# Performance work log

Hardware: AMD Instinct MI355X
Metric: run time of the kernel (lower is better)

The kernel has to match this reference:

```python
import jax, jax.numpy as jnp
import numpy as np

EPS = 1e-08


def setup_inputs() -> dict:
    key = jax.random.key(0)
    k_x, k_w1, k_b1, k_w2, k_b2 = jax.random.split(key, 5)
    B, C, T = 64, 64, 4000
    x = jax.random.normal(k_x, (B, C, T, 1), dtype=jnp.float32)
    # 1x1 Conv2D with in_channels=1, out_channels=8 -> weight is an 8-vector + bias
    w1 = jax.random.normal(k_w1, (8,), dtype=jnp.float32) * 0.5
    b1 = jax.random.normal(k_b1, (8,), dtype=jnp.float32) * 0.1
    w2 = jax.random.normal(k_w2, (8,), dtype=jnp.float32) * 0.5
    b2 = jax.random.normal(k_b2, (8,), dtype=jnp.float32) * 0.1
    # gamma is initialized to 0 in the module (residual identity at init);
    # use a nonzero value so the attention path is exercised numerically.
    gamma = jnp.float32(0.5)
    return {"x": x, "w1": w1, "b1": b1, "w2": w2, "b2": b2, "gamma": gamma}


def reference(x, w1, b1, w2, b2, gamma):
    B, C, T, _ = x.shape  # (B, num_ch, T, 1)
    # 1x1 conv with C_in=1: broadcast multiply-add, then flatten (T, 8) -> T*8
    q = (x * w1 + b1).reshape(B, C, T * 8)  # proj_query (B, C, T*8)
    k = (x * w2 + b2).reshape(B, C, T * 8)  # proj_key   (B, C, T*8)
    # energy = Q @ K^T  -> (B, C, C)
    energy = jnp.einsum('bcd,bed->bce', q, k)
    # custom min-max normalization along last axis, then softmax
    max_h = jnp.max(energy, axis=2, keepdims=True)
    min_h = jnp.min(energy, axis=2, keepdims=True)
    energy = (energy - min_h) / (max_h - min_h + EPS)
    attention = jax.nn.softmax(energy, axis=-1)
    xs = x[..., 0]  # squeeze last dim -> (B, C, T)
    # attention^T @ xs  (transpose_a=True)
    attended = jnp.einsum('bec,bet->bct', attention, xs)
    return gamma * attended[..., None] + x
```

## Files before the change

kernel.cpp:

```cpp
#include <hip/hip_runtime.h>

#define BB 64
#define CC 64
#define TT 4000

#define SLABS 8
#define TSLAB 250
#define SLABT (2 * TSLAB)
#define GP_PITCH 264

#define TPB 128
#define APITCH 72

#define GPART_ELEMS ((size_t)SLABS * BB * CC * CC)

typedef short short8 __attribute__((ext_vector_type(8)));
typedef float f32x16 __attribute__((ext_vector_type(16)));

__device__ __forceinline__ short f2bf(float f) {
    unsigned u = __float_as_uint(f);
    u = (u + 0x7FFFu + ((u >> 16) & 1u)) >> 16;
    return (short)u;
}
__device__ __forceinline__ float bfpair(unsigned u) {
    return __uint_as_float(u << 16) + __uint_as_float(u & 0xFFFF0000u);
}

__device__ __forceinline__ void stage_load(const float* __restrict__ xb, int t0,
                                           int g, int tid, float4 v[8]) {
    #pragma unroll
    for (int k = 0; k < 8; ++k) {
        const int i = tid + 256 * (g * 8 + k);
        const int row = i >> 6, tq = i & 63;
        float4 w = make_float4(0.f, 0.f, 0.f, 0.f);
        if (tq < 62) {
            w = *(const float4*)(xb + row * TT + t0 + 4 * tq);
        } else if (tq == 62) {
            const float* p = xb + row * TT + t0 + 248;
            w.x = p[0]; w.y = p[1];
        }
        v[k] = w;
    }
}
__device__ __forceinline__ void stage_write(short* xs, int g, int tid, const float4 v[8]) {
    #pragma unroll
    for (int k = 0; k < 8; ++k) {
        const int i = tid + 256 * (g * 8 + k);
        const int row = i >> 6, tq = i & 63;
        short4 sv;
        sv.x = f2bf(v[k].x); sv.y = f2bf(v[k].y);
        sv.z = f2bf(v[k].z); sv.w = f2bf(v[k].w);
        const int pc = (tq >> 1) ^ (row & 7);
        *(short4*)(xs + row * GP_PITCH + pc * 8 + (tq & 1) * 4) = sv;
    }
}
__device__ __forceinline__ float s_partial(const short* xs, int lane, int wave) {
    const short* rowp = xs + lane * GP_PITCH;
    float s = 0.f;
    #pragma unroll
    for (int j = 0; j < 8; ++j) {
        const int pc = (wave * 8 + j) ^ (lane & 7);
        uint2 u0 = *(const uint2*)(rowp + pc * 8);
        uint2 u1 = *(const uint2*)(rowp + pc * 8 + 4);
        s += bfpair(u0.x) + bfpair(u0.y) + bfpair(u1.x) + bfpair(u1.y);
    }
    return s;
}
__device__ __forceinline__ void mfma_tile(const short* xs, int r0, int c0,
                                          int m, int half, f32x16& acc) {
    #pragma unroll
    for (int ks = 0; ks < 16; ++ks) {
        const int ck = ks * 2 + half;
        short8 av = *(const short8*)(xs + (r0 + m) * GP_PITCH + (ck ^ (m & 7)) * 8);
        short8 bv = *(const short8*)(xs + (c0 + m) * GP_PITCH + (ck ^ (m & 7)) * 8);
        acc = __builtin_amdgcn_mfma_f32_32x32x16_bf16(av, bv, acc, 0, 0, 0);
    }
}

__global__ __launch_bounds__(256)
void gram_mfma(const float* __restrict__ x, float* __restrict__ G_part,
               float* __restrict__ S_part) {
    __shared__ short xs[2][CC * GP_PITCH];
    __shared__ float sred[4 * 64];
    const int b    = blockIdx.x / SLABS;
    const int slab = blockIdx.x % SLABS;
    const int tid  = threadIdx.x;
    const int lane = tid & 63;
    const int wave = tid >> 6;
    const float* xb = x + (size_t)b * CC * TT;

    const int r0 = (wave >> 1) * 32, c0 = (wave & 1) * 32;
    const int m = lane & 31, half = lane >> 5;
    f32x16 acc;
    #pragma unroll
    for (int z = 0; z < 16; ++z) acc[z] = 0.f;

    const int t0a = slab * SLABT, t0b = t0a + TSLAB;

    {
        float4 v[8];
        stage_load(xb, t0a, 0, tid, v);
        stage_write(xs[0], 0, tid, v);
        stage_load(xb, t0a, 1, tid, v);
        stage_write(xs[0], 1, tid, v);
    }
    __syncthreads();

    float4 p0[8], p1[8];
    stage_load(xb, t0b, 0, tid, p0);
    stage_load(xb, t0b, 1, tid, p1);

    float s_acc = s_partial(xs[0], lane, wave);
    mfma_tile(xs[0], r0, c0, m, half, acc);

    stage_write(xs[1], 0, tid, p0);
    stage_write(xs[1], 1, tid, p1);
    __syncthreads();

    s_acc += s_partial(xs[1], lane, wave);
    mfma_tile(xs[1], r0, c0, m, half, acc);

    sred[wave * 64 + lane] = s_acc;
    __syncthreads();
    if (tid < 64) {
        float s = sred[tid] + sred[64 + tid] + sred[128 + tid] + sred[192 + tid];
        S_part[(slab * BB + b) * CC + tid] = s;
    }
    float* gp = G_part + ((size_t)slab * BB + b) * (CC * CC);
    #pragma unroll
    for (int r = 0; r < 16; ++r) {
        const int row = (r & 3) + 8 * (r >> 2) + 4 * half;
        gp[(r0 + row) * CC + (c0 + m)] = acc[r];
    }
}

__global__ __launch_bounds__(256)
void softmax_apply(const float* __restrict__ x,
                   const float* __restrict__ w1, const float* __restrict__ b1,
                   const float* __restrict__ w2, const float* __restrict__ b2,
                   const float* __restrict__ G_part, const float* __restrict__ S_part,
                   const float* __restrict__ gamma, float* __restrict__ out) {
    __shared__ float Es[64 * 65];
    __shared__ short al[CC * APITCH];
    __shared__ float red[3 * 256];
    __shared__ float Sb[64];
    const int tid  = threadIdx.x;
    const int lane = tid & 63, wave = tid >> 6;
    const int b    = blockIdx.x & 63;
    const int slab = blockIdx.x >> 6;
    const float* xb = x + (size_t)b * CC * TT;
    const int m = lane & 31, half = lane >> 5;

    {
        #pragma unroll
        for (int j4 = 0; j4 < 4; ++j4) {
            const int jj = tid + 256 * j4;
            float4 s = make_float4(0.f, 0.f, 0.f, 0.f);
            #pragma unroll
            for (int sl = 0; sl < SLABS; ++sl) {
                const float4 g = *(const float4*)(G_part + ((size_t)sl * BB + b) * 4096 + 4 * jj);
                s.x += g.x; s.y += g.y; s.z += g.z; s.w += g.w;
            }
            const int row = jj >> 4, col = (jj & 15) * 4;
            float* e = Es + row * 65 + col;
            e[0] = s.x; e[1] = s.y; e[2] = s.z; e[3] = s.w;
        }
        if (tid < 64) {
            float s = 0.f;
            #pragma unroll
            for (int sl = 0; sl < SLABS; ++sl)
                s += S_part[(sl * BB + b) * CC + tid];
            Sb[tid] = s;
        }
        float A = 0.f, Bc = 0.f, Be = 0.f, Cc = 0.f;
        #pragma unroll
        for (int j = 0; j < 8; ++j) {
            float a1 = w1[j], a2 = w2[j], q1 = b1[j], q2 = b2[j];
            A += a1 * a2; Bc += a1 * q2; Be += q1 * a2; Cc += q1 * q2;
        }
        Cc *= (float)TT;
        __syncthreads();

        const int c = tid & 63, q = tid >> 6;
        const float sc = Sb[c];
        float ev[16], mn = 1e30f, mx = -1e30f;
        #pragma unroll
        for (int i = 0; i < 16; ++i) {
            const int e = 16 * q + i;
            float en = A * Es[c * 65 + e] + Bc * sc + Be * Sb[e] + Cc;
            ev[i] = en;
            mn = fminf(mn, en); mx = fmaxf(mx, en);
        }
        red[q * 64 + c] = mn; red[256 + q * 64 + c] = mx;
        __syncthreads();
        mn = fminf(fminf(red[c], red[64 + c]), fminf(red[128 + c], red[192 + c]));
        mx = fmaxf(fmaxf(red[256 + c], red[320 + c]), fmaxf(red[384 + c], red[448 + c]));
        const float ninv = 1.f / (mx - mn + 1e-8f);
        float pv[16], ls = 0.f;
        #pragma unroll
        for (int i = 0; i < 16; ++i) {
            float p = __expf((ev[i] - mn) * ninv);
            pv[i] = p; ls += p;
        }
        red[512 + q * 64 + c] = ls;
        __syncthreads();
        const float rinv = 1.f / (red[512 + c] + red[576 + c] + red[640 + c] + red[704 + c]);
        #pragma unroll
        for (int i = 0; i < 16; ++i)
            al[(16 * q + i) * APITCH + c] = f2bf(pv[i] * rinv);
        __syncthreads();
    }

    {
        const int c0 = (wave & 1) * 32;
        const int tb = (wave >> 1) * 64;
        short8 av[4];
        #pragma unroll
        for (int ks = 0; ks < 4; ++ks)
            av[ks] = *(const short8*)(al + (c0 + m) * APITCH + ks * 16 + 8 * half);

        const float gm = gamma[0];
        float* ob = out + (size_t)b * CC * TT;
        const int t0s = slab * SLABT;

        for (int it = 0; it < 4; ++it) {
            const int t0 = t0s + it * TPB;
            const int ta = t0 + tb + m;
            const int tc = ta + 32;
            f32x16 acc0, acc1;
            #pragma unroll
            for (int z = 0; z < 16; ++z) { acc0[z] = 0.f; acc1[z] = 0.f; }

            #pragma unroll
            for (int ks = 0; ks < 4; ++ks) {
                const int eb = ks * 16 + 8 * half;
                short8 bv0, bv1;
                #pragma unroll
                for (int j = 0; j < 8; ++j) {
                    const float xa = (ta < TT) ? xb[(eb + j) * TT + ta] : 0.f;
                    const float xc = (tc < TT) ? xb[(eb + j) * TT + tc] : 0.f;
                    bv0[j] = f2bf(xa);
                    bv1[j] = f2bf(xc);
                }
                acc0 = __builtin_amdgcn_mfma_f32_32x32x16_bf16(av[ks], bv0, acc0, 0, 0, 0);
                acc1 = __builtin_amdgcn_mfma_f32_32x32x16_bf16(av[ks], bv1, acc1, 0, 0, 0);
            }

            const int tl0 = it * TPB + tb + m;
            #pragma unroll
            for (int r = 0; r < 16; ++r) {
                const int row = (r & 3) + 8 * (r >> 2) + 4 * half;
                const int c = c0 + row;
                if (tl0 < SLABT)
                    ob[c * TT + ta] = gm * acc0[r] + xb[c * TT + ta];
                if (tl0 + 32 < SLABT)
                    ob[c * TT + tc] = gm * acc1[r] + xb[c * TT + tc];
            }
        }
    }
}

extern "C" void kernel_launch(void* const* d_in, const int* in_sizes, int n_in,
                              void* d_out, int out_size, void* d_ws, size_t ws_size,
                              hipStream_t stream) {
    const float* x  = (const float*)d_in[0];
    const float* w1 = (const float*)d_in[1];
    const float* b1 = (const float*)d_in[2];
    const float* w2 = (const float*)d_in[3];
    const float* b2 = (const float*)d_in[4];
    const float* gm = (const float*)d_in[5];
    float* out = (float*)d_out;

    float* G_part = (float*)d_ws;
    float* S_part = G_part + GPART_ELEMS;

    hipLaunchKernelGGL(gram_mfma, dim3(BB * SLABS), dim3(256), 0, stream,
                       x, G_part, S_part);
    hipLaunchKernelGGL(softmax_apply, dim3(BB * SLABS), dim3(256), 0, stream,
                       x, w1, b1, w2, b2, G_part, S_part, gm, out);
}
```

Baseline: 184.3 us.

## Stage x tiles in LDS with register prefetch and packed bf16 conversion

Result: faster. 157.3 us (-14.7%).

```diff
diff --git a/kernel.cpp b/kernel.cpp
--- a/kernel.cpp
+++ b/kernel.cpp
@@ -10,17 +10,24 @@
 #define GP_PITCH 264
 
 #define TPB 128
+#define XPITCH 132
 #define APITCH 72
 
 #define GPART_ELEMS ((size_t)SLABS * BB * CC * CC)
 
 typedef short short8 __attribute__((ext_vector_type(8)));
 typedef float f32x16 __attribute__((ext_vector_type(16)));
+typedef unsigned u32x4 __attribute__((ext_vector_type(4)));
 
 __device__ __forceinline__ short f2bf(float f) {
     unsigned u = __float_as_uint(f);
     u = (u + 0x7FFFu + ((u >> 16) & 1u)) >> 16;
     return (short)u;
+}
+__device__ __forceinline__ unsigned cvt_pk(float a, float b) {
+    unsigned r;
+    asm("v_cvt_pk_bf16_f32 %0, %1, %2" : "=v"(r) : "v"(a), "v"(b));
+    return r;
 }
 __device__ __forceinline__ float bfpair(unsigned u) {
     return __uint_as_float(u << 16) + __uint_as_float(u & 0xFFFF0000u);
@@ -47,11 +54,11 @@
     for (int k = 0; k < 8; ++k) {
         const int i = tid + 256 * (g * 8 + k);
         const int row = i >> 6, tq = i & 63;
-        short4 sv;
-        sv.x = f2bf(v[k].x); sv.y = f2bf(v[k].y);
-        sv.z = f2bf(v[k].z); sv.w = f2bf(v[k].w);
+        uint2 sv;
+        sv.x = cvt_pk(v[k].x, v[k].y);
+        sv.y = cvt_pk(v[k].z, v[k].w);
         const int pc = (tq >> 1) ^ (row & 7);
-        *(short4*)(xs + row * GP_PITCH + pc * 8 + (tq & 1) * 4) = sv;
+        *(uint2*)(xs + row * GP_PITCH + pc * 8 + (tq & 1) * 4) = sv;
     }
 }
 __device__ __forceinline__ float s_partial(const short* xs, int lane, int wave) {
@@ -141,6 +148,7 @@
                    const float* __restrict__ G_part, const float* __restrict__ S_part,
                    const float* __restrict__ gamma, float* __restrict__ out) {
     __shared__ float Es[64 * 65];
+    __shared__ float xsbuf[CC * XPITCH];
     __shared__ short al[CC * APITCH];
     __shared__ float red[3 * 256];
     __shared__ float Sb[64];
@@ -222,40 +230,70 @@
         const float gm = gamma[0];
         float* ob = out + (size_t)b * CC * TT;
         const int t0s = slab * SLABT;
+        const int ie = tid >> 5, ip = tid & 31;
+
+        float4 v[8];
+        #pragma unroll
+        for (int k = 0; k < 8; ++k) {
+            const int i = tid + 256 * k;
+            const int e = i >> 5, p = i & 31;
+            const int t = t0s + 4 * p;
+            v[k] = make_float4(0.f, 0.f, 0.f, 0.f);
+            if (t < TT) v[k] = *(const float4*)(xb + e * TT + t);
+        }
 
         for (int it = 0; it < 4; ++it) {
-            const int t0 = t0s + it * TPB;
-            const int ta = t0 + tb + m;
-            const int tc = ta + 32;
+            #pragma unroll
+            for (int k = 0; k < 8; ++k) {
+                const int i = tid + 256 * k;
+                const int e = i >> 5, p = i & 31;
+                *(float4*)(xsbuf + e * XPITCH + 4 * p) = v[k];
+            }
+            __syncthreads();
+            if (it < 3) {
+                const int t0n = t0s + (it + 1) * TPB;
+                #pragma unroll
+                for (int k = 0; k < 8; ++k) {
+                    const int i = tid + 256 * k;
+                    const int e = i >> 5, p = i & 31;
+                    const int t = t0n + 4 * p;
+                    v[k] = make_float4(0.f, 0.f, 0.f, 0.f);
+                    if (t < TT) v[k] = *(const float4*)(xb + e * TT + t);
+                }
+            }
+
             f32x16 acc0, acc1;
             #pragma unroll
             for (int z = 0; z < 16; ++z) { acc0[z] = 0.f; acc1[z] = 0.f; }
-
             #pragma unroll
             for (int ks = 0; ks < 4; ++ks) {
                 const int eb = ks * 16 + 8 * half;
-                short8 bv0, bv1;
+                u32x4 pk0, pk1;
                 #pragma unroll
-                for (int j = 0; j < 8; ++j) {
-                    const float xa = (ta < TT) ? xb[(eb + j) * TT + ta] : 0.f;
-                    const float xc = (tc < TT) ? xb[(eb + j) * TT + tc] : 0.f;
-                    bv0[j] = f2bf(xa);
-                    bv1[j] = f2bf(xc);
+                for (int j2 = 0; j2 < 4; ++j2) {
+                    const float* col = xsbuf + (eb + 2 * j2) * XPITCH;
+                    pk0[j2] = cvt_pk(col[tb + m],      col[XPITCH + tb + m]);
+                    pk1[j2] = cvt_pk(col[tb + 32 + m], col[XPITCH + tb + 32 + m]);
                 }
-                acc0 = __builtin_amdgcn_mfma_f32_32x32x16_bf16(av[ks], bv0, acc0, 0, 0, 0);
-                acc1 = __builtin_amdgcn_mfma_f32_32x32x16_bf16(av[ks], bv1, acc1, 0, 0, 0);
-            }
-
+                acc0 = __builtin_amdgcn_mfma_f32_32x32x16_bf16(
+                    av[ks], __builtin_bit_cast(short8, pk0), acc0, 0, 0, 0);
+                acc1 = __builtin_amdgcn_mfma_f32_32x32x16_bf16(
+                    av[ks], __builtin_bit_cast(short8, pk1), acc1, 0, 0, 0);
+            }
+
+            const int t0  = t0s + it * TPB;
+            const int ta  = t0 + tb + m, tc = ta + 32;
             const int tl0 = it * TPB + tb + m;
             #pragma unroll
             for (int r = 0; r < 16; ++r) {
                 const int row = (r & 3) + 8 * (r >> 2) + 4 * half;
                 const int c = c0 + row;
                 if (tl0 < SLABT)
-                    ob[c * TT + ta] = gm * acc0[r] + xb[c * TT + ta];
+                    ob[c * TT + ta] = gm * acc0[r] + xsbuf[c * XPITCH + tb + m];
                 if (tl0 + 32 < SLABT)
-                    ob[c * TT + tc] = gm * acc1[r] + xb[c * TT + tc];
-            }
+                    ob[c * TT + tc] = gm * acc1[r] + xsbuf[c * XPITCH + tb + 32 + m];
+            }
+            __syncthreads();
         }
     }
 }
```

## Fuse Gram, softmax and apply into one kernel with redundant per-block Gram

Applied to the files above, without the earlier changes.

After: 361.4 us. 96.1% more time.

```diff
diff --git a/kernel.cpp b/kernel.cpp
--- a/kernel.cpp
+++ b/kernel.cpp
@@ -4,15 +4,11 @@
 #define CC 64
 #define TT 4000
 
-#define SLABS 8
-#define TSLAB 250
-#define SLABT (2 * TSLAB)
+#define NSLAB 8
+#define NCHUNK 16
+#define TCH 250
 #define GP_PITCH 264
-
-#define TPB 128
 #define APITCH 72
-
-#define GPART_ELEMS ((size_t)SLABS * BB * CC * CC)
 
 typedef short short8 __attribute__((ext_vector_type(8)));
 typedef float f32x16 __attribute__((ext_vector_type(16)));
@@ -22,8 +18,16 @@
     u = (u + 0x7FFFu + ((u >> 16) & 1u)) >> 16;
     return (short)u;
 }
+__device__ __forceinline__ unsigned cvt_pk(float a, float b) {
+    unsigned r;
+    asm("v_cvt_pk_bf16_f32 %0, %1, %2" : "=v"(r) : "v"(a), "v"(b));
+    return r;
+}
 __device__ __forceinline__ float bfpair(unsigned u) {
     return __uint_as_float(u << 16) + __uint_as_float(u & 0xFFFF0000u);
+}
+__device__ __forceinline__ float bf2f(short s) {
+    return __uint_as_float(((unsigned)(unsigned short)s) << 16);
 }
 
 __device__ __forceinline__ void stage_load(const float* __restrict__ xb, int t0,
@@ -47,11 +51,11 @@
     for (int k = 0; k < 8; ++k) {
         const int i = tid + 256 * (g * 8 + k);
         const int row = i >> 6, tq = i & 63;
-        short4 sv;
-        sv.x = f2bf(v[k].x); sv.y = f2bf(v[k].y);
-        sv.z = f2bf(v[k].z); sv.w = f2bf(v[k].w);
+        uint2 sv;
+        sv.x = cvt_pk(v[k].x, v[k].y);
+        sv.y = cvt_pk(v[k].z, v[k].w);
         const int pc = (tq >> 1) ^ (row & 7);
-        *(short4*)(xs + row * GP_PITCH + pc * 8 + (tq & 1) * 4) = sv;
+        *(uint2*)(xs + row * GP_PITCH + pc * 8 + (tq & 1) * 4) = sv;
     }
 }
 __device__ __forceinline__ float s_partial(const short* xs, int lane, int wave) {
@@ -78,100 +82,59 @@
 }
 
 __global__ __launch_bounds__(256)
-void gram_mfma(const float* __restrict__ x, float* __restrict__ G_part,
-               float* __restrict__ S_part) {
-    __shared__ short xs[2][CC * GP_PITCH];
-    __shared__ float sred[4 * 64];
-    const int b    = blockIdx.x / SLABS;
-    const int slab = blockIdx.x % SLABS;
-    const int tid  = threadIdx.x;
-    const int lane = tid & 63;
-    const int wave = tid >> 6;
-    const float* xb = x + (size_t)b * CC * TT;
-
-    const int r0 = (wave >> 1) * 32, c0 = (wave & 1) * 32;
-    const int m = lane & 31, half = lane >> 5;
-    f32x16 acc;
-    #pragma unroll
-    for (int z = 0; z < 16; ++z) acc[z] = 0.f;
-
-    const int t0a = slab * SLABT, t0b = t0a + TSLAB;
-
-    {
-        float4 v[8];
-        stage_load(xb, t0a, 0, tid, v);
-        stage_write(xs[0], 0, tid, v);
-        stage_load(xb, t0a, 1, tid, v);
-        stage_write(xs[0], 1, tid, v);
-    }
-    __syncthreads();
-
-    float4 p0[8], p1[8];
-    stage_load(xb, t0b, 0, tid, p0);
-    stage_load(xb, t0b, 1, tid, p1);
-
-    float s_acc = s_partial(xs[0], lane, wave);
-    mfma_tile(xs[0], r0, c0, m, half, acc);
-
-    stage_write(xs[1], 0, tid, p0);
-    stage_write(xs[1], 1, tid, p1);
-    __syncthreads();
-
-    s_acc += s_partial(xs[1], lane, wave);
-    mfma_tile(xs[1], r0, c0, m, half, acc);
-
-    sred[wave * 64 + lane] = s_acc;
-    __syncthreads();
-    if (tid < 64) {
-        float s = sred[tid] + sred[64 + tid] + sred[128 + tid] + sred[192 + tid];
-        S_part[(slab * BB + b) * CC + tid] = s;
-    }
-    float* gp = G_part + ((size_t)slab * BB + b) * (CC * CC);
-    #pragma unroll
-    for (int r = 0; r < 16; ++r) {
-        const int row = (r & 3) + 8 * (r >> 2) + 4 * half;
-        gp[(r0 + row) * CC + (c0 + m)] = acc[r];
-    }
-}
-
-__global__ __launch_bounds__(256)
-void softmax_apply(const float* __restrict__ x,
-                   const float* __restrict__ w1, const float* __restrict__ b1,
-                   const float* __restrict__ w2, const float* __restrict__ b2,
-                   const float* __restrict__ G_part, const float* __restrict__ S_part,
-                   const float* __restrict__ gamma, float* __restrict__ out) {
+void fused_ca(const float* __restrict__ x,
+              const float* __restrict__ w1, const float* __restrict__ b1,
+              const float* __restrict__ w2, const float* __restrict__ b2,
+              const float* __restrict__ gamma, float* __restrict__ out) {
+    __shared__ short buf[CC * GP_PITCH];
     __shared__ float Es[64 * 65];
     __shared__ short al[CC * APITCH];
     __shared__ float red[3 * 256];
     __shared__ float Sb[64];
+
     const int tid  = threadIdx.x;
     const int lane = tid & 63, wave = tid >> 6;
     const int b    = blockIdx.x & 63;
     const int slab = blockIdx.x >> 6;
     const float* xb = x + (size_t)b * CC * TT;
     const int m = lane & 31, half = lane >> 5;
+    const int r0 = (wave >> 1) * 32, c0w = (wave & 1) * 32;
+
+    f32x16 acc;
+    #pragma unroll
+    for (int z = 0; z < 16; ++z) acc[z] = 0.f;
+    float s_acc = 0.f;
+
+    float4 v0[8], v1[8];
+    stage_load(xb, 0, 0, tid, v0);
+    stage_load(xb, 0, 1, tid, v1);
+    for (int ch = 0; ch < NCHUNK; ++ch) {
+        stage_write(buf, 0, tid, v0);
+        stage_write(buf, 1, tid, v1);
+        __syncthreads();
+        if (ch < NCHUNK - 1) {
+            stage_load(xb, (ch + 1) * TCH, 0, tid, v0);
+            stage_load(xb, (ch + 1) * TCH, 1, tid, v1);
+        }
+        s_acc += s_partial(buf, lane, wave);
+        mfma_tile(buf, r0, c0w, m, half, acc);
+        __syncthreads();
+    }
+
+    stage_load(xb, (2 * slab) * TCH, 0, tid, v0);
+    stage_load(xb, (2 * slab) * TCH, 1, tid, v1);
+
+    red[wave * 64 + lane] = s_acc;
+    #pragma unroll
+    for (int r = 0; r < 16; ++r) {
+        const int row = (r & 3) + 8 * (r >> 2) + 4 * half;
+        Es[(r0 + row) * 65 + (c0w + m)] = acc[r];
+    }
+    __syncthreads();
+    if (tid < 64)
+        Sb[tid] = red[tid] + red[64 + tid] + red[128 + tid] + red[192 + tid];
 
     {
-        #pragma unroll
-        for (int j4 = 0; j4 < 4; ++j4) {
-            const int jj = tid + 256 * j4;
-            float4 s = make_float4(0.f, 0.f, 0.f, 0.f);
-            #pragma unroll
-            for (int sl = 0; sl < SLABS; ++sl) {
-                const float4 g = *(const float4*)(G_part + ((size_t)sl * BB + b) * 4096 + 4 * jj);
-                s.x += g.x; s.y += g.y; s.z += g.z; s.w += g.w;
-            }
-            const int row = jj >> 4, col = (jj & 15) * 4;
-            float* e = Es + row * 65 + col;
-            e[0] = s.x; e[1] = s.y; e[2] = s.z; e[3] = s.w;
-        }
-        if (tid < 64) {
-            float s = 0.f;
-            #pragma unroll
-            for (int sl = 0; sl < SLABS; ++sl)
-                s += S_part[(sl * BB + b) * CC + tid];
-            Sb[tid] = s;
-        }
         float A = 0.f, Bc = 0.f, Be = 0.f, Cc = 0.f;
         #pragma unroll
         for (int j = 0; j < 8; ++j) {
@@ -181,7 +144,7 @@
         Cc *= (float)TT;
         __syncthreads();
 
-        const int c = tid & 63, q = tid >> 6;
+        const int c = lane, q = wave;
         const float sc = Sb[c];
         float ev[16], mn = 1e30f, mx = -1e30f;
         #pragma unroll
@@ -208,54 +171,65 @@
         #pragma unroll
         for (int i = 0; i < 16; ++i)
             al[(16 * q + i) * APITCH + c] = f2bf(pv[i] * rinv);
-        __syncthreads();
-    }
+    }
+    __syncthreads();
 
     {
-        const int c0 = (wave & 1) * 32;
+        const float gm = gamma[0];
+        float* ob = out + (size_t)b * CC * TT;
         const int tb = (wave >> 1) * 64;
         short8 av[4];
         #pragma unroll
         for (int ks = 0; ks < 4; ++ks)
-            av[ks] = *(const short8*)(al + (c0 + m) * APITCH + ks * 16 + 8 * half);
-
-        const float gm = gamma[0];
-        float* ob = out + (size_t)b * CC * TT;
-        const int t0s = slab * SLABT;
-
-        for (int it = 0; it < 4; ++it) {
-            const int t0 = t0s + it * TPB;
-            const int ta = t0 + tb + m;
-            const int tc = ta + 32;
-            f32x16 acc0, acc1;
+            av[ks] = *(const short8*)(al + (c0w + m) * APITCH + ks * 16 + 8 * half);
+
+        for (int hr = 0; hr < 2; ++hr) {
+            stage_write(buf, 0, tid, v0);
+            stage_write(buf, 1, tid, v1);
+            __syncthreads();
+            if (hr == 0) {
+                stage_load(xb, (2 * slab + 1) * TCH, 0, tid, v0);
+                stage_load(xb, (2 * slab + 1) * TCH, 1, tid, v1);
+            }
+            const int tg0 = (2 * slab + hr) * TCH;
+
             #pragma unroll
-            for (int z = 0; z < 16; ++z) { acc0[z] = 0.f; acc1[z] = 0.f; }
-
-            #pragma unroll
-            for (int ks = 0; ks < 4; ++ks) {
-                const int eb = ks * 16 + 8 * half;
-                short8 bv0, bv1;
+            for (int it = 0; it < 2; ++it) {
+                const int tl0 = it * 128 + tb + m;
+                const int tl1 = tl0 + 32;
+                const int tq0 = tl0 >> 3, tq1 = tl1 >> 3, el = tl0 & 7;
+                f32x16 acc0, acc1;
                 #pragma unroll
-                for (int j = 0; j < 8; ++j) {
-                    const float xa = (ta < TT) ? xb[(eb + j) * TT + ta] : 0.f;
-                    const float xc = (tc < TT) ? xb[(eb + j) * TT + tc] : 0.f;
-                    bv0[j] = f2bf(xa);
-                    bv1[j] = f2bf(xc);
+                for (int z = 0; z < 16; ++z) { acc0[z] = 0.f; acc1[z] = 0.f; }
+
+                #pragma unroll
+                for (int ks = 0; ks < 4; ++ks) {
+                    short8 bv0, bv1;
+                    #pragma unroll
+                    for (int j = 0; j < 8; ++j) {
+                        const int e = ks * 16 + 8 * half + j;
+                        const short* rp = buf + e * GP_PITCH;
+                        bv0[j] = rp[((tq0 ^ (e & 7)) << 3) + el];
+                        bv1[j] = rp[((tq1 ^ (e & 7)) << 3) + el];
+                    }
+                    acc0 = __builtin_amdgcn_mfma_f32_32x32x16_bf16(av[ks], bv0, acc0, 0, 0, 0);
+                    acc1 = __builtin_amdgcn_mfma_f32_32x32x16_bf16(av[ks], bv1, acc1, 0, 0, 0);
                 }
-                acc0 = __builtin_amdgcn_mfma_f32_32x32x16_bf16(av[ks], bv0, acc0, 0, 0, 0);
-                acc1 = __builtin_amdgcn_mfma_f32_32x32x16_bf16(av[ks], bv1, acc1, 0, 0, 0);
+
+                #pragma unroll
+                for (int r = 0; r < 16; ++r) {
+                    const int row = (r & 3) + 8 * (r >> 2) + 4 * half;
+                    const int cch = c0w + row;
+                    const short* rp = buf + cch * GP_PITCH;
+                    if (tl0 < TCH)
+                        ob[cch * TT + tg0 + tl0] =
+                            gm * acc0[r] + bf2f(rp[((tq0 ^ (cch & 7)) << 3) + el]);
+                    if (tl1 < TCH)
+                        ob[cch * TT + tg0 + tl1] =
+                            gm * acc1[r] + bf2f(rp[((tq1 ^ (cch & 7)) << 3) + el]);
+                }
             }
-
-            const int tl0 = it * TPB + tb + m;
-            #pragma unroll
-            for (int r = 0; r < 16; ++r) {
-                const int row = (r & 3) + 8 * (r >> 2) + 4 * half;
-                const int c = c0 + row;
-                if (tl0 < SLABT)
-                    ob[c * TT + ta] = gm * acc0[r] + xb[c * TT + ta];
-                if (tl0 + 32 < SLABT)
-                    ob[c * TT + tc] = gm * acc1[r] + xb[c * TT + tc];
-            }
+            if (hr == 0) __syncthreads();
         }
     }
 }
@@ -271,11 +245,6 @@
     const float* gm = (const float*)d_in[5];
     float* out = (float*)d_out;
 
-    float* G_part = (float*)d_ws;
-    float* S_part = G_part + GPART_ELEMS;
-
-    hipLaunchKernelGGL(gram_mfma, dim3(BB * SLABS), dim3(256), 0, stream,
-                       x, G_part, S_part);
-    hipLaunchKernelGGL(softmax_apply, dim3(BB * SLABS), dim3(256), 0, stream,
-                       x, w1, b1, w2, b2, G_part, S_part, gm, out);
-}
+    hipLaunchKernelGGL(fused_ca, dim3(BB * NSLAB), dim3(256), 0, stream,
+                       x, w1, b1, w2, b2, gm, out);
+}
```
